# Kernel optimization log

Hardware: AMD Instinct MI355X
Metric: run time of the kernel (lower is better)

The kernel has to match this reference:

```python
import jax, jax.numpy as jnp
import numpy as np

N_USERS = 50000
N_ITEMS = 40000
D = 64
E = 1_000_000
NB = 3       # behaviors
L = 2        # GCN layers per behavior
B = 8192
N_NODES = (N_USERS + 1) + (N_ITEMS + 1)
REG_WEIGHT = 0.01
CL_TEMP = 0.1
BPR_GAMMA = 1e-10


def setup_inputs() -> dict:
    key = jax.random.key(0)
    k1, k2, k3, k4, k5 = jax.random.split(key, 5)
    user_emb = jax.random.normal(k1, (N_USERS + 1, D), jnp.float32) * 0.1
    item_emb = jax.random.normal(k2, (N_ITEMS + 1, D), jnp.float32) * 0.1
    gcn_w = jax.random.normal(k3, (NB, L, D, D), jnp.float32) * 0.1
    gcn_b = jnp.zeros((NB, L, D), jnp.float32)
    edge_index = jax.random.randint(k4, (NB, 2, E), 0, N_NODES, dtype=jnp.int64)
    batch_data = jax.random.randint(k5, (B, NB, 3), 0, 40000, dtype=jnp.int64)
    return {"user_emb": user_emb, "item_emb": item_emb, "gcn_w": gcn_w,
            "gcn_b": gcn_b, "edge_index": edge_index, "batch_data": batch_data}


def gcn_layer(x, edge_index, W, b):
    # PyG GCNConv(add_self_loops=False): h = x @ W; out[col] += norm * h[row]; out += b
    row, col = edge_index[0], edge_index[1]
    n = x.shape[0]
    deg = jnp.zeros((n,), x.dtype).at[col].add(1.0)
    dinv = jnp.where(deg > 0, jax.lax.rsqrt(jnp.maximum(deg, 1.0)), 0.0)
    norm = dinv[row] * dinv[col]                    # [E]
    h = x @ W                                       # [N, D]
    msg = h[row] * norm[:, None]                    # [E, D] gather
    out = jnp.zeros_like(x).at[col].add(msg)        # scatter-add
    return out + b


def _cos(a, b):
    num = jnp.sum(a * b, axis=-1)
    den = jnp.maximum(jnp.linalg.norm(a, axis=-1) * jnp.linalg.norm(b, axis=-1), 1e-8)
    return num / den


def reference(user_emb, item_emb, gcn_w, gcn_b, edge_index, batch_data):
    total = jnp.concatenate([user_emb, item_emb], axis=0)   # [N_NODES, D]
    total_loss = jnp.float32(0.0)
    te = total
    for bi in range(NB):
        # gcn propagate for this behavior (eval: dropout is identity)
        le = te
        for l in range(L):
            le = gcn_layer(le, edge_index[bi], gcn_w[bi, l], gcn_b[bi, l])
        # F.normalize(dim=-1)
        le = le / jnp.maximum(jnp.linalg.norm(le, axis=-1, keepdims=True), 1e-12)
        te = le + te
        # losses for this behavior
        users = batch_data[:, bi, 0]
        items = batch_data[:, bi, 1:]                        # [B, 2]
        ue = te[:N_USERS + 1]
        ie = te[N_USERS + 1:]
        uf = ue[users]                                       # [B, D]
        itf = ie[items]                                      # [B, 2, D]
        pos, neg = itf[:, 0], itf[:, 1]
        # info-nce (cross-entropy over [pos, neg] cosine sims, label 0)
        logits = jnp.stack([_cos(uf, pos), _cos(uf, neg)], axis=1) / CL_TEMP
        cl_loss = jnp.mean(-jax.nn.log_softmax(logits, axis=-1)[:, 0])
        # BPR loss (weight per behavior = 1.0)
        scores = jnp.sum(uf[:, None, :] * itf, axis=2)       # [B, 2]
        bpr = jnp.mean(-jnp.log(BPR_GAMMA + jax.nn.sigmoid(scores[:, 0] - scores[:, 1])))
        total_loss = total_loss + bpr + cl_loss
    # EmbLoss: sum of L2 norms of the raw embedding tables / last table's rows
    emb_loss = (jnp.linalg.norm(user_emb) + jnp.linalg.norm(item_emb)) / item_emb.shape[0]
    return total_loss + REG_WEIGHT * emb_loss
```

## Files before the change

### kernel.cpp

```cpp
#include <hip/hip_runtime.h>
#include <hip/hip_fp16.h>
#include <math.h>

#define NU 50001
#define NI 40001
#define NNODES 90002
#define DD 64
#define EE 1000000
#define NBB 3
#define LL 2
#define BB 8192
#define STRIDE 40
#define QS 16.0f
#define T4U (NU * 16)
#define T4T (NNODES * 16)
#define NBIN 352
#define NPAD (NBIN * 256)
#define CHUNK 4096
#define NBLK 245

__global__ __launch_bounds__(512) void k_scatp(const int* __restrict__ edge,
                                               unsigned* __restrict__ binbufC,
                                               unsigned* __restrict__ Hcnt,
                                               unsigned* __restrict__ Hoff) {
    __shared__ unsigned posc[NBIN];
    __shared__ unsigned sc[512];
    __shared__ unsigned lb[CHUNK];
    int bi = blockIdx.y, blk = blockIdx.x, tid = threadIdx.x;
    for (int i = tid; i < NBIN; i += 512) posc[i] = 0;
    __syncthreads();
    const int* rowp = edge + (size_t)bi * 2 * EE;
    const int* colp = rowp + EE;
    int base = blk * CHUNK;
    unsigned pk[8], bn[8];
    #pragma unroll
    for (int k = 0; k < 8; k++) {
        int e = base + k * 512 + tid;
        if (e < EE) {
            unsigned c = (unsigned)colp[e];
            pk[k] = ((c & 255u) << 17) | (unsigned)rowp[e];
            bn[k] = c >> 8;
            atomicAdd(&posc[bn[k]], 1u);
        } else bn[k] = 0xFFFFFFFFu;
    }
    __syncthreads();
    unsigned v = (tid < NBIN) ? posc[tid] : 0u;
    sc[tid] = v;
    __syncthreads();
    #pragma unroll
    for (int o = 1; o < 512; o <<= 1) {
        unsigned u = (tid >= o) ? sc[tid - o] : 0u;
        __syncthreads();
        sc[tid] += u;
        __syncthreads();
    }
    if (tid < NBIN) {
        unsigned excl = sc[tid] - v;
        Hcnt[((size_t)bi * NBLK + blk) * NBIN + tid] = v;
        Hoff[((size_t)bi * NBLK + blk) * NBIN + tid] = excl;
        posc[tid] = excl;
    }
    __syncthreads();
    #pragma unroll
    for (int k = 0; k < 8; k++) {
        if (bn[k] != 0xFFFFFFFFu) {
            unsigned pos = atomicAdd(&posc[bn[k]], 1u);
            lb[pos] = pk[k];
        }
    }
    __syncthreads();
    uint4* d4 = (uint4*)(binbufC + ((size_t)bi * NBLK + blk) * CHUNK);
    const uint4* s4 = (const uint4*)lb;
    #pragma unroll
    for (int k = 0; k < CHUNK / 4 / 512; k++)
        d4[k * 512 + tid] = s4[k * 512 + tid];
}

__global__ __launch_bounds__(256) void k_bucket(const unsigned* __restrict__ Hcnt,
                                                const unsigned* __restrict__ Hoff,
                                                const unsigned* __restrict__ binbufC,
                                                unsigned* __restrict__ cnt3, unsigned* __restrict__ bucket3) {
    __shared__ unsigned lb[256 * STRIDE];
    __shared__ unsigned cl[256];
    __shared__ unsigned so[NBLK + 1];
    __shared__ unsigned bo[NBLK];
    __shared__ unsigned sc[256];
    int bi = blockIdx.y, bin = blockIdx.x, tid = threadIdx.x;
    cl[tid] = 0;
    unsigned v = 0;
    if (tid < NBLK) {
        v = Hcnt[((size_t)bi * NBLK + tid) * NBIN + bin];
        bo[tid] = Hoff[((size_t)bi * NBLK + tid) * NBIN + bin];
    }
    sc[tid] = v;
    __syncthreads();
    #pragma unroll
    for (int o = 1; o < 256; o <<= 1) {
        unsigned u = (tid >= o) ? sc[tid - o] : 0u;
        __syncthreads();
        sc[tid] += u;
        __syncthreads();
    }
    if (tid == 0) so[0] = 0;
    if (tid < NBLK) so[tid + 1] = sc[tid];
    __syncthreads();
    unsigned T = so[NBLK];
    for (unsigned i = tid; i < T; i += 256) {
        int lo = 0, hi = NBLK;
        while (hi - lo > 1) { int mid = (lo + hi) >> 1; if (so[mid] <= i) lo = mid; else hi = mid; }
        unsigned w = binbufC[((size_t)bi * NBLK + lo) * CHUNK + bo[lo] + (i - so[lo])];
        unsigned c = w >> 17;
        unsigned pos = atomicAdd(&cl[c], 1u);
        if (pos < STRIDE) lb[c * STRIDE + pos] = w & 0x1FFFFu;
    }
    __syncthreads();
    cnt3[(size_t)bi * NPAD + (size_t)bin * 256 + tid] = cl[tid];
    uint4* dst = (uint4*)(bucket3 + (size_t)bi * NPAD * STRIDE + (size_t)bin * 256 * STRIDE);
    const uint4* srcl = (const uint4*)lb;
    #pragma unroll
    for (int k = 0; k < (256 * STRIDE / 4) / 256; k++)
        dst[k * 256 + tid] = srcl[k * 256 + tid];
}

__global__ __launch_bounds__(256) void k_init(const float* __restrict__ user_emb,
                                              const float* __restrict__ item_emb,
                                              const unsigned* __restrict__ cnt0,
                                              float* __restrict__ te, unsigned* __restrict__ X8a,
                                              float* __restrict__ scal) {
    int i0 = blockIdx.x * 256 + threadIdx.x;
    int stride = gridDim.x * 256;
    float su = 0.f, si = 0.f;
    const float4* u4 = (const float4*)user_emb;
    const float4* i4 = (const float4*)item_emb;
    float4* t4 = (float4*)te;
    for (int i = i0; i < T4T; i += stride) {
        float4 v;
        if (i < T4U) { v = u4[i]; su += v.x * v.x + v.y * v.y + v.z * v.z + v.w * v.w; }
        else         { v = i4[i - T4U]; si += v.x * v.x + v.y * v.y + v.z * v.z + v.w * v.w; }
        t4[i] = v;
        unsigned d = cnt0[i >> 4];
        float q = (d ? rsqrtf((float)d) : 0.f) * QS;
        int p0 = __builtin_amdgcn_cvt_pk_fp8_f32(v.x * q, v.y * q, 0, false);
        p0 = __builtin_amdgcn_cvt_pk_fp8_f32(v.z * q, v.w * q, p0, true);
        X8a[i] = (unsigned)p0;
    }
    #pragma unroll
    for (int o = 32; o > 0; o >>= 1) { su += __shfl_down(su, o); si += __shfl_down(si, o); }
    __shared__ float lsu[4], lsi[4];
    int w = threadIdx.x >> 6;
    if ((threadIdx.x & 63) == 0) { lsu[w] = su; lsi[w] = si; }
    __syncthreads();
    if (threadIdx.x == 0) {
        atomicAdd(scal + 1, lsu[0] + lsu[1] + lsu[2] + lsu[3]);
        atomicAdd(scal + 2, lsi[0] + lsi[1] + lsi[2] + lsi[3]);
    }
}

__global__ __launch_bounds__(256) void k_agg(const unsigned* __restrict__ cnt,
                                             const unsigned* __restrict__ bucket,
                                             const uint2* __restrict__ X8in,
                                             __half* __restrict__ agg) {
    int t = blockIdx.x * 256 + threadIdx.x;
    int r = t >> 6;
    if (r >= NNODES) return;
    int lane = t & 63;
    int j2 = lane & 7;
    int hw = lane >> 3;
    unsigned d = cnt[r];
    unsigned dc = d < STRIDE ? d : STRIDE;
    const unsigned* bk = bucket + (size_t)r * STRIDE;
    unsigned a0 = (hw +  0 < dc) ? bk[hw +  0] : (unsigned)NNODES;
    unsigned a1 = (hw +  8 < dc) ? bk[hw +  8] : (unsigned)NNODES;
    unsigned a2 = (hw + 16 < dc) ? bk[hw + 16] : (unsigned)NNODES;
    unsigned a3 = (hw + 24 < dc) ? bk[hw + 24] : (unsigned)NNODES;
    uint2 w0 = X8in[(size_t)a0 * 8 + j2];
    uint2 w1 = X8in[(size_t)a1 * 8 + j2];
    uint2 w2 = X8in[(size_t)a2 * 8 + j2];
    uint2 w3 = X8in[(size_t)a3 * 8 + j2];
    float4 A = {0.f, 0.f, 0.f, 0.f}, Bv = {0.f, 0.f, 0.f, 0.f};
#define ACC8(W) { \
    A.x  += __builtin_amdgcn_cvt_f32_fp8((int)W.x, 0); \
    A.y  += __builtin_amdgcn_cvt_f32_fp8((int)W.x, 1); \
    A.z  += __builtin_amdgcn_cvt_f32_fp8((int)W.x, 2); \
    A.w  += __builtin_amdgcn_cvt_f32_fp8((int)W.x, 3); \
    Bv.x += __builtin_amdgcn_cvt_f32_fp8((int)W.y, 0); \
    Bv.y += __builtin_amdgcn_cvt_f32_fp8((int)W.y, 1); \
    Bv.z += __builtin_amdgcn_cvt_f32_fp8((int)W.y, 2); \
    Bv.w += __builtin_amdgcn_cvt_f32_fp8((int)W.y, 3); }
    ACC8(w0) ACC8(w1) ACC8(w2) ACC8(w3)
    for (unsigned i = hw + 32; i < dc; i += 8) {
        uint2 w = X8in[(size_t)bk[i] * 8 + j2];
        ACC8(w)
    }
#undef ACC8
    #pragma unroll
    for (int o = 8; o <= 32; o <<= 1) {
        A.x  += __shfl_xor(A.x, o);  A.y  += __shfl_xor(A.y, o);
        A.z  += __shfl_xor(A.z, o);  A.w  += __shfl_xor(A.w, o);
        Bv.x += __shfl_xor(Bv.x, o); Bv.y += __shfl_xor(Bv.y, o);
        Bv.z += __shfl_xor(Bv.z, o); Bv.w += __shfl_xor(Bv.w, o);
    }
    if (hw == 0) {
        union { __half2 h[4]; float4 f; } u;
        u.h[0] = __floats2half2_rn(A.x, A.y);
        u.h[1] = __floats2half2_rn(A.z, A.w);
        u.h[2] = __floats2half2_rn(Bv.x, Bv.y);
        u.h[3] = __floats2half2_rn(Bv.z, Bv.w);
        ((float4*)agg)[(size_t)r * 8 + j2] = u.f;
    }
}

template <int FUSE>
__global__ __launch_bounds__(256) void k_gemmE(const __half* __restrict__ agg, const float* __restrict__ W,
                                               const float* __restrict__ b, const unsigned* __restrict__ cnt,
                                               float* __restrict__ te, unsigned* __restrict__ X8out,
                                               const unsigned* __restrict__ cnt_next) {
    __shared__ float ws[64 * 64];
    __shared__ float xs[16][64];
    int tid = threadIdx.x;
    #pragma unroll
    for (int q = 0; q < 4; q++)
        ((float4*)ws)[tid + q * 256] = ((const float4*)W)[tid + q * 256];
    int r0 = blockIdx.x * 16;
    {
        int rr = r0 + (tid >> 4);
        int cc = (tid & 15) * 4;
        if (rr < NNODES) {
            uint2 u = ((const uint2*)agg)[(size_t)rr * 16 + (tid & 15)];
            union { unsigned u; __half2 h; } c0, c1;
            c0.u = u.x; c1.u = u.y;
            float2 f0 = __half22float2(c0.h);
            float2 f1 = __half22float2(c1.h);
            xs[tid >> 4][cc + 0] = f0.x; xs[tid >> 4][cc + 1] = f0.y;
            xs[tid >> 4][cc + 2] = f1.x; xs[tid >> 4][cc + 3] = f1.y;
        }
    }
    __syncthreads();
    int rloc = tid >> 4;
    int j = tid & 15;
    int d4 = j * 4;
    int row = r0 + rloc;
    if (row >= NNODES) return;
    float4 acc = {0.f, 0.f, 0.f, 0.f};
    #pragma unroll
    for (int k = 0; k < 64; k++) {
        float xv = xs[rloc][k];
        float4 wv = *(const float4*)&ws[k * 64 + d4];
        acc.x += xv * wv.x; acc.y += xv * wv.y;
        acc.z += xv * wv.z; acc.w += xv * wv.w;
    }
    unsigned d = cnt[row];
    float m = (d ? rsqrtf((float)d) : 0.f) * (1.0f / QS);
    float4 bb = ((const float4*)b)[j];
    float vx = acc.x * m + bb.x;
    float vy = acc.y * m + bb.y;
    float vz = acc.z * m + bb.z;
    float vw = acc.w * m + bb.w;
    if (FUSE == 0) {
        unsigned dn = cnt_next[row];
        float q = (dn ? rsqrtf((float)dn) : 0.f) * QS;
        int p0 = __builtin_amdgcn_cvt_pk_fp8_f32(vx * q, vy * q, 0, false);
        p0 = __builtin_amdgcn_cvt_pk_fp8_f32(vz * q, vw * q, p0, true);
        X8out[(size_t)row * 16 + j] = (unsigned)p0;
    } else {
        float s = vx * vx + vy * vy + vz * vz + vw * vw;
        #pragma unroll
        for (int o = 1; o <= 8; o <<= 1) s += __shfl_xor(s, o);
        float scale = 1.f / fmaxf(sqrtf(s), 1e-12f);
        float4* te4 = (float4*)te;
        float4 old = te4[(size_t)row * 16 + j];
        old.x += vx * scale; old.y += vy * scale;
        old.z += vz * scale; old.w += vw * scale;
        te4[(size_t)row * 16 + j] = old;
        if (X8out) {
            unsigned dn = cnt_next[row];
            float q = (dn ? rsqrtf((float)dn) : 0.f) * QS;
            int p0 = __builtin_amdgcn_cvt_pk_fp8_f32(old.x * q, old.y * q, 0, false);
            p0 = __builtin_amdgcn_cvt_pk_fp8_f32(old.z * q, old.w * q, p0, true);
            X8out[(size_t)row * 16 + j] = (unsigned)p0;
        }
    }
}

__global__ __launch_bounds__(256) void k_loss(const float* __restrict__ te, const int* __restrict__ batch,
                                              int bi, float* __restrict__ acc) {
    int t = blockIdx.x * 256 + threadIdx.x;
    int s = t >> 6;
    int lane = t & 63;
    if (s >= BB) return;
    const int* bd = &batch[s * (NBB * 3) + bi * 3];
    int u = bd[0], p = bd[1], n = bd[2];
    float uv = te[(size_t)u * DD + lane];
    float pv = te[(size_t)(NU + p) * DD + lane];
    float nv = te[(size_t)(NU + n) * DD + lane];
    float d_up = uv * pv, d_un = uv * nv;
    float s_u = uv * uv, s_p = pv * pv, s_n = nv * nv;
    for (int o = 32; o > 0; o >>= 1) {
        d_up += __shfl_xor(d_up, o);
        d_un += __shfl_xor(d_un, o);
        s_u  += __shfl_xor(s_u, o);
        s_p  += __shfl_xor(s_p, o);
        s_n  += __shfl_xor(s_n, o);
    }
    __shared__ float part[4];
    if (lane == 0) {
        float cosp = d_up / fmaxf(sqrtf(s_u) * sqrtf(s_p), 1e-8f);
        float cosn = d_un / fmaxf(sqrtf(s_u) * sqrtf(s_n), 1e-8f);
        float cl = log1pf(expf((cosn - cosp) * 10.0f));
        float sig = 1.f / (1.f + expf(-(d_up - d_un)));
        float bpr = -logf(1e-10f + sig);
        part[(threadIdx.x >> 6) & 3] = cl + bpr;
    }
    __syncthreads();
    if (threadIdx.x == 0)
        atomicAdd(acc, (part[0] + part[1] + part[2] + part[3]) * (1.0f / BB));
}

__global__ void k_final(const float* __restrict__ scal, float* __restrict__ out) {
    if (threadIdx.x == 0 && blockIdx.x == 0)
        out[0] = scal[0] + 0.01f * (sqrtf(scal[1]) + sqrtf(scal[2])) / 40001.0f;
}

extern "C" void kernel_launch(void* const* d_in, const int* in_sizes, int n_in,
                              void* d_out, int out_size, void* d_ws, size_t ws_size,
                              hipStream_t stream) {
    const float* user_emb = (const float*)d_in[0];
    const float* item_emb = (const float*)d_in[1];
    const float* gcn_w    = (const float*)d_in[2];
    const float* gcn_b    = (const float*)d_in[3];
    const int*   edge_idx = (const int*)d_in[4];
    const int*   batch    = (const int*)d_in[5];
    float* out = (float*)d_out;

    char* ws = (char*)d_ws;
    size_t off = 0;
    auto alloc = [&](size_t bytes) {
        void* p = ws + off;
        off = (off + bytes + 511) & ~(size_t)511;
        return p;
    };
    float*    te      = (float*)alloc((size_t)NNODES * DD * sizeof(float));
    __half*   agg     = (__half*)alloc((size_t)NNODES * DD * sizeof(__half));
    unsigned* X8a     = (unsigned*)alloc((size_t)(NNODES + 1) * 16 * sizeof(unsigned));
    unsigned* X8b     = (unsigned*)alloc((size_t)(NNODES + 1) * 16 * sizeof(unsigned));
    unsigned* cnt3    = (unsigned*)alloc((size_t)NBB * NPAD * sizeof(unsigned));
    unsigned* bucket3 = (unsigned*)alloc((size_t)NBB * NPAD * STRIDE * sizeof(unsigned));
    unsigned* binbufC = (unsigned*)alloc((size_t)NBB * NBLK * CHUNK * sizeof(unsigned));
    unsigned* Hcnt    = (unsigned*)alloc((size_t)NBB * NBLK * NBIN * sizeof(unsigned));
    unsigned* Hoff    = (unsigned*)alloc((size_t)NBB * NBLK * NBIN * sizeof(unsigned));
    float*    scal    = (float*)alloc(64 * sizeof(float));

    hipMemsetAsync(scal, 0, 64 * sizeof(float), stream);
    hipMemsetAsync(X8a + (size_t)NNODES * 16, 0, 64, stream);
    hipMemsetAsync(X8b + (size_t)NNODES * 16, 0, 64, stream);

    k_scatp <<<dim3(NBLK, NBB), 512, 0, stream>>>(edge_idx, binbufC, Hcnt, Hoff);
    k_bucket<<<dim3(NBIN, NBB), 256, 0, stream>>>(Hcnt, Hoff, binbufC, cnt3, bucket3);

    k_init<<<1024, 256, 0, stream>>>(user_emb, item_emb, cnt3, te, X8a, scal);

    const int gat_grid  = (NNODES * DD + 255) / 256;
    const int gemm_grid = (NNODES + 15) / 16;

    for (int bi = 0; bi < NBB; bi++) {
        const unsigned* cnt = cnt3 + (size_t)bi * NPAD;
        const unsigned* bucket = bucket3 + (size_t)bi * NPAD * STRIDE;
        const float* W0 = gcn_w + ((size_t)bi * LL + 0) * DD * DD;
        const float* b0 = gcn_b + ((size_t)bi * LL + 0) * DD;
        const float* W1 = gcn_w + ((size_t)bi * LL + 1) * DD * DD;
        const float* b1 = gcn_b + ((size_t)bi * LL + 1) * DD;

        k_agg<<<gat_grid, 256, 0, stream>>>(cnt, bucket, (const uint2*)X8a, agg);
        k_gemmE<0><<<gemm_grid, 256, 0, stream>>>(agg, W0, b0, cnt, nullptr, X8b, cnt);

        k_agg<<<gat_grid, 256, 0, stream>>>(cnt, bucket, (const uint2*)X8b, agg);
        unsigned* x8next = (bi < NBB - 1) ? X8a : nullptr;
        const unsigned* cnt_next = cnt3 + (size_t)((bi + 1) % NBB) * NPAD;
        k_gemmE<1><<<gemm_grid, 256, 0, stream>>>(agg, W1, b1, cnt, te, x8next, cnt_next);

        k_loss<<<(BB * 64) / 256, 256, 0, stream>>>(te, batch, bi, scal);
    }

    k_final<<<1, 64, 0, stream>>>(scal, out);
}
```

Baseline: 485.4 us.

## Fold two GCN layer weights into one GEMM and transpose histogram table

Because the propagation operator is linear, the two per-behavior layer weights are premultiplied (W0·W1) and the layer-0 bias is carried through the second aggregation as a per-row dinv-weighted sum times b0·W1. This removes one GEMM kernel per behavior: the first aggregation now writes fp8 directly at a new quantisation scale. A transpose kernel is added so the bucket kernel reads its histogram coalesced, and small precompute kernels build dinv and the fused weights. The risks are extra fp8 rounding error from the different scaling and the cost of several added small launches.

```diff
diff --git a/kernel.cpp b/kernel.cpp
--- a/kernel.cpp
+++ b/kernel.cpp
@@ -12,6 +12,7 @@
 #define BB 8192
 #define STRIDE 40
 #define QS 16.0f
+#define QS2 64.0f
 #define T4U (NU * 16)
 #define T4T (NNODES * 16)
 #define NBIN 352
@@ -19,10 +20,20 @@
 #define CHUNK 4096
 #define NBLK 245
 
+__device__ __forceinline__ void acc8(float4& A, float4& Bv, uint2 w) {
+    A.x  += __builtin_amdgcn_cvt_f32_fp8((int)w.x, 0);
+    A.y  += __builtin_amdgcn_cvt_f32_fp8((int)w.x, 1);
+    A.z  += __builtin_amdgcn_cvt_f32_fp8((int)w.x, 2);
+    A.w  += __builtin_amdgcn_cvt_f32_fp8((int)w.x, 3);
+    Bv.x += __builtin_amdgcn_cvt_f32_fp8((int)w.y, 0);
+    Bv.y += __builtin_amdgcn_cvt_f32_fp8((int)w.y, 1);
+    Bv.z += __builtin_amdgcn_cvt_f32_fp8((int)w.y, 2);
+    Bv.w += __builtin_amdgcn_cvt_f32_fp8((int)w.y, 3);
+}
+
 __global__ __launch_bounds__(512) void k_scatp(const int* __restrict__ edge,
                                                unsigned* __restrict__ binbufC,
-                                               unsigned* __restrict__ Hcnt,
-                                               unsigned* __restrict__ Hoff) {
+                                               unsigned* __restrict__ Htab) {
     __shared__ unsigned posc[NBIN];
     __shared__ unsigned sc[512];
     __shared__ unsigned lb[CHUNK];
@@ -56,8 +67,8 @@
     }
     if (tid < NBIN) {
         unsigned excl = sc[tid] - v;
-        Hcnt[((size_t)bi * NBLK + blk) * NBIN + tid] = v;
-        Hoff[((size_t)bi * NBLK + blk) * NBIN + tid] = excl;
+        Htab[(((size_t)bi * 2 + 0) * NBLK + blk) * NBIN + tid] = v;
+        Htab[(((size_t)bi * 2 + 1) * NBLK + blk) * NBIN + tid] = excl;
         posc[tid] = excl;
     }
     __syncthreads();
@@ -76,8 +87,21 @@
         d4[k * 512 + tid] = s4[k * 512 + tid];
 }
 
-__global__ __launch_bounds__(256) void k_bucket(const unsigned* __restrict__ Hcnt,
-                                                const unsigned* __restrict__ Hoff,
+__global__ __launch_bounds__(1024) void k_transp(const unsigned* __restrict__ in, unsigned* __restrict__ out) {
+    __shared__ unsigned t[32][33];
+    int z = blockIdx.z;
+    const unsigned* I = in + (size_t)z * NBLK * NBIN;
+    unsigned* O = out + (size_t)z * NBIN * NBLK;
+    int bin0 = blockIdx.x * 32, blk0 = blockIdx.y * 32;
+    int tx = threadIdx.x & 31, ty = threadIdx.x >> 5;
+    int bin = bin0 + tx, blk = blk0 + ty;
+    if (blk < NBLK && bin < NBIN) t[ty][tx] = I[(size_t)blk * NBIN + bin];
+    __syncthreads();
+    int obin = bin0 + ty, oblk = blk0 + tx;
+    if (obin < NBIN && oblk < NBLK) O[(size_t)obin * NBLK + oblk] = t[tx][ty];
+}
+
+__global__ __launch_bounds__(256) void k_bucket(const unsigned* __restrict__ HtabT,
                                                 const unsigned* __restrict__ binbufC,
                                                 unsigned* __restrict__ cnt3, unsigned* __restrict__ bucket3) {
     __shared__ unsigned lb[256 * STRIDE];
@@ -89,8 +113,8 @@
     cl[tid] = 0;
     unsigned v = 0;
     if (tid < NBLK) {
-        v = Hcnt[((size_t)bi * NBLK + tid) * NBIN + bin];
-        bo[tid] = Hoff[((size_t)bi * NBLK + tid) * NBIN + bin];
+        v = HtabT[(((size_t)bi * 2 + 0) * NBIN + bin) * NBLK + tid];
+        bo[tid] = HtabT[(((size_t)bi * 2 + 1) * NBIN + bin) * NBLK + tid];
     }
     sc[tid] = v;
     __syncthreads();
@@ -120,6 +144,44 @@
     #pragma unroll
     for (int k = 0; k < (256 * STRIDE / 4) / 256; k++)
         dst[k * 256 + tid] = srcl[k * 256 + tid];
+}
+
+__global__ __launch_bounds__(256) void k_dinv3(const unsigned* __restrict__ cnt3, float* __restrict__ dinv3) {
+    int i = blockIdx.x * 256 + threadIdx.x;
+    if (i < NBB * NPAD) { unsigned d = cnt3[i]; dinv3[i] = d ? rsqrtf((float)d) : 0.f; }
+}
+
+__global__ __launch_bounds__(256) void k_wprep(const float* __restrict__ gcn_w, const float* __restrict__ gcn_b,
+                                               float* __restrict__ W01, float* __restrict__ bW) {
+    __shared__ float w0[64 * 64], w1[64 * 64];
+    int bi = blockIdx.x, tid = threadIdx.x;
+    const float* W0 = gcn_w + ((size_t)bi * 2 + 0) * 4096;
+    const float* W1 = gcn_w + ((size_t)bi * 2 + 1) * 4096;
+    #pragma unroll
+    for (int k = 0; k < 4; k++) {
+        ((float4*)w0)[k * 256 + tid] = ((const float4*)W0)[k * 256 + tid];
+        ((float4*)w1)[k * 256 + tid] = ((const float4*)W1)[k * 256 + tid];
+    }
+    __syncthreads();
+    int i = tid & 63;
+    int jq = tid >> 6;
+    float acc[16];
+    #pragma unroll
+    for (int j = 0; j < 16; j++) acc[j] = 0.f;
+    for (int k = 0; k < 64; k++) {
+        float a = w0[i * 64 + k];
+        #pragma unroll
+        for (int j = 0; j < 16; j++) acc[j] += a * w1[k * 64 + jq * 16 + j];
+    }
+    float* O = W01 + (size_t)bi * 4096 + (size_t)i * 64 + jq * 16;
+    #pragma unroll
+    for (int j = 0; j < 16; j++) O[j] = acc[j];
+    if (tid < 64) {
+        const float* b0 = gcn_b + ((size_t)bi * 2 + 0) * 64;
+        float a = 0.f;
+        for (int k = 0; k < 64; k++) a += b0[k] * w1[k * 64 + tid];
+        bW[bi * 64 + tid] = a;
+    }
 }
 
 __global__ __launch_bounds__(256) void k_init(const float* __restrict__ user_emb,
@@ -153,6 +215,59 @@
     if (threadIdx.x == 0) {
         atomicAdd(scal + 1, lsu[0] + lsu[1] + lsu[2] + lsu[3]);
         atomicAdd(scal + 2, lsi[0] + lsi[1] + lsi[2] + lsi[3]);
+    }
+}
+
+__global__ __launch_bounds__(256) void k_agg1(const unsigned* __restrict__ cnt,
+                                              const unsigned* __restrict__ bucket,
+                                              const uint2* __restrict__ X8in,
+                                              const float* __restrict__ dinv,
+                                              unsigned* __restrict__ X8out,
+                                              float* __restrict__ sarr) {
+    int t = blockIdx.x * 256 + threadIdx.x;
+    int r = t >> 6;
+    if (r >= NNODES) return;
+    int lane = t & 63;
+    int j2 = lane & 7;
+    int hw = lane >> 3;
+    unsigned d = cnt[r];
+    unsigned dc = d < STRIDE ? d : STRIDE;
+    const unsigned* bk = bucket + (size_t)r * STRIDE;
+    unsigned a0 = (hw +  0 < dc) ? bk[hw +  0] : (unsigned)NNODES;
+    unsigned a1 = (hw +  8 < dc) ? bk[hw +  8] : (unsigned)NNODES;
+    unsigned a2 = (hw + 16 < dc) ? bk[hw + 16] : (unsigned)NNODES;
+    unsigned a3 = (hw + 24 < dc) ? bk[hw + 24] : (unsigned)NNODES;
+    uint2 w0 = X8in[(size_t)a0 * 8 + j2];
+    uint2 w1 = X8in[(size_t)a1 * 8 + j2];
+    uint2 w2 = X8in[(size_t)a2 * 8 + j2];
+    uint2 w3 = X8in[(size_t)a3 * 8 + j2];
+    float sa = dinv[a0] + dinv[a1] + dinv[a2] + dinv[a3];
+    float4 A = {0.f, 0.f, 0.f, 0.f}, Bv = {0.f, 0.f, 0.f, 0.f};
+    acc8(A, Bv, w0); acc8(A, Bv, w1); acc8(A, Bv, w2); acc8(A, Bv, w3);
+    for (unsigned i = hw + 32; i < dc; i += 8) {
+        unsigned a = bk[i];
+        uint2 w = X8in[(size_t)a * 8 + j2];
+        acc8(A, Bv, w);
+        sa += dinv[a];
+    }
+    #pragma unroll
+    for (int o = 8; o <= 32; o <<= 1) {
+        A.x  += __shfl_xor(A.x, o);  A.y  += __shfl_xor(A.y, o);
+        A.z  += __shfl_xor(A.z, o);  A.w  += __shfl_xor(A.w, o);
+        Bv.x += __shfl_xor(Bv.x, o); Bv.y += __shfl_xor(Bv.y, o);
+        Bv.z += __shfl_xor(Bv.z, o); Bv.w += __shfl_xor(Bv.w, o);
+        sa   += __shfl_xor(sa, o);
+    }
+    float dv = dinv[r];
+    if (hw == 0) {
+        float q2 = QS2 * dv * dv * (1.0f / QS);
+        int p0 = __builtin_amdgcn_cvt_pk_fp8_f32(A.x * q2, A.y * q2, 0, false);
+        p0 = __builtin_amdgcn_cvt_pk_fp8_f32(A.z * q2, A.w * q2, p0, true);
+        int p1 = __builtin_amdgcn_cvt_pk_fp8_f32(Bv.x * q2, Bv.y * q2, 0, false);
+        p1 = __builtin_amdgcn_cvt_pk_fp8_f32(Bv.z * q2, Bv.w * q2, p1, true);
+        uint2 pw; pw.x = (unsigned)p0; pw.y = (unsigned)p1;
+        ((uint2*)X8out)[(size_t)r * 8 + j2] = pw;
+        if (j2 == 0) sarr[r] = dv * sa;
     }
 }
 
@@ -178,21 +293,11 @@
     uint2 w2 = X8in[(size_t)a2 * 8 + j2];
     uint2 w3 = X8in[(size_t)a3 * 8 + j2];
     float4 A = {0.f, 0.f, 0.f, 0.f}, Bv = {0.f, 0.f, 0.f, 0.f};
-#define ACC8(W) { \
-    A.x  += __builtin_amdgcn_cvt_f32_fp8((int)W.x, 0); \
-    A.y  += __builtin_amdgcn_cvt_f32_fp8((int)W.x, 1); \
-    A.z  += __builtin_amdgcn_cvt_f32_fp8((int)W.x, 2); \
-    A.w  += __builtin_amdgcn_cvt_f32_fp8((int)W.x, 3); \
-    Bv.x += __builtin_amdgcn_cvt_f32_fp8((int)W.y, 0); \
-    Bv.y += __builtin_amdgcn_cvt_f32_fp8((int)W.y, 1); \
-    Bv.z += __builtin_amdgcn_cvt_f32_fp8((int)W.y, 2); \
-    Bv.w += __builtin_amdgcn_cvt_f32_fp8((int)W.y, 3); }
-    ACC8(w0) ACC8(w1) ACC8(w2) ACC8(w3)
+    acc8(A, Bv, w0); acc8(A, Bv, w1); acc8(A, Bv, w2); acc8(A, Bv, w3);
     for (unsigned i = hw + 32; i < dc; i += 8) {
         uint2 w = X8in[(size_t)bk[i] * 8 + j2];
-        ACC8(w)
-    }
-#undef ACC8
+        acc8(A, Bv, w);
+    }
     #pragma unroll
     for (int o = 8; o <= 32; o <<= 1) {
         A.x  += __shfl_xor(A.x, o);  A.y  += __shfl_xor(A.y, o);
@@ -210,9 +315,9 @@
     }
 }
 
-template <int FUSE>
-__global__ __launch_bounds__(256) void k_gemmE(const __half* __restrict__ agg, const float* __restrict__ W,
-                                               const float* __restrict__ b, const unsigned* __restrict__ cnt,
+__global__ __launch_bounds__(256) void k_gemmE(const __half* __restrict__ agg, const float* __restrict__ W01,
+                                               const float* __restrict__ bW, const float* __restrict__ b1,
+                                               const unsigned* __restrict__ cnt, const float* __restrict__ sarr,
                                                float* __restrict__ te, unsigned* __restrict__ X8out,
                                                const unsigned* __restrict__ cnt_next) {
     __shared__ float ws[64 * 64];
@@ -220,7 +325,7 @@
     int tid = threadIdx.x;
     #pragma unroll
     for (int q = 0; q < 4; q++)
-        ((float4*)ws)[tid + q * 256] = ((const float4*)W)[tid + q * 256];
+        ((float4*)ws)[tid + q * 256] = ((const float4*)W01)[tid + q * 256];
     int r0 = blockIdx.x * 16;
     {
         int rr = r0 + (tid >> 4);
@@ -250,35 +355,29 @@
         acc.z += xv * wv.z; acc.w += xv * wv.w;
     }
     unsigned d = cnt[row];
-    float m = (d ? rsqrtf((float)d) : 0.f) * (1.0f / QS);
-    float4 bb = ((const float4*)b)[j];
-    float vx = acc.x * m + bb.x;
-    float vy = acc.y * m + bb.y;
-    float vz = acc.z * m + bb.z;
-    float vw = acc.w * m + bb.w;
-    if (FUSE == 0) {
+    float m = (d ? rsqrtf((float)d) : 0.f) * (1.0f / QS2);
+    float sv = sarr[row];
+    float4 bwv = ((const float4*)bW)[j];
+    float4 b1v = ((const float4*)b1)[j];
+    float vx = acc.x * m + sv * bwv.x + b1v.x;
+    float vy = acc.y * m + sv * bwv.y + b1v.y;
+    float vz = acc.z * m + sv * bwv.z + b1v.z;
+    float vw = acc.w * m + sv * bwv.w + b1v.w;
+    float s = vx * vx + vy * vy + vz * vz + vw * vw;
+    #pragma unroll
+    for (int o = 1; o <= 8; o <<= 1) s += __shfl_xor(s, o);
+    float scale = 1.f / fmaxf(sqrtf(s), 1e-12f);
+    float4* te4 = (float4*)te;
+    float4 old = te4[(size_t)row * 16 + j];
+    old.x += vx * scale; old.y += vy * scale;
+    old.z += vz * scale; old.w += vw * scale;
+    te4[(size_t)row * 16 + j] = old;
+    if (X8out) {
         unsigned dn = cnt_next[row];
         float q = (dn ? rsqrtf((float)dn) : 0.f) * QS;
-        int p0 = __builtin_amdgcn_cvt_pk_fp8_f32(vx * q, vy * q, 0, false);
-        p0 = __builtin_amdgcn_cvt_pk_fp8_f32(vz * q, vw * q, p0, true);
+        int p0 = __builtin_amdgcn_cvt_pk_fp8_f32(old.x * q, old.y * q, 0, false);
+        p0 = __builtin_amdgcn_cvt_pk_fp8_f32(old.z * q, old.w * q, p0, true);
         X8out[(size_t)row * 16 + j] = (unsigned)p0;
-    } else {
-        float s = vx * vx + vy * vy + vz * vz + vw * vw;
-        #pragma unroll
-        for (int o = 1; o <= 8; o <<= 1) s += __shfl_xor(s, o);
-        float scale = 1.f / fmaxf(sqrtf(s), 1e-12f);
-        float4* te4 = (float4*)te;
-        float4 old = te4[(size_t)row * 16 + j];
-        old.x += vx * scale; old.y += vy * scale;
-        old.z += vz * scale; old.w += vw * scale;
-        te4[(size_t)row * 16 + j] = old;
-        if (X8out) {
-            unsigned dn = cnt_next[row];
-            float q = (dn ? rsqrtf((float)dn) : 0.f) * QS;
-            int p0 = __builtin_amdgcn_cvt_pk_fp8_f32(old.x * q, old.y * q, 0, false);
-            p0 = __builtin_amdgcn_cvt_pk_fp8_f32(old.z * q, old.w * q, p0, true);
-            X8out[(size_t)row * 16 + j] = (unsigned)p0;
-        }
     }
 }
 
@@ -344,18 +443,25 @@
     unsigned* X8a     = (unsigned*)alloc((size_t)(NNODES + 1) * 16 * sizeof(unsigned));
     unsigned* X8b     = (unsigned*)alloc((size_t)(NNODES + 1) * 16 * sizeof(unsigned));
     unsigned* cnt3    = (unsigned*)alloc((size_t)NBB * NPAD * sizeof(unsigned));
+    float*    dinv3   = (float*)alloc((size_t)NBB * NPAD * sizeof(float));
     unsigned* bucket3 = (unsigned*)alloc((size_t)NBB * NPAD * STRIDE * sizeof(unsigned));
     unsigned* binbufC = (unsigned*)alloc((size_t)NBB * NBLK * CHUNK * sizeof(unsigned));
-    unsigned* Hcnt    = (unsigned*)alloc((size_t)NBB * NBLK * NBIN * sizeof(unsigned));
-    unsigned* Hoff    = (unsigned*)alloc((size_t)NBB * NBLK * NBIN * sizeof(unsigned));
+    unsigned* Htab    = (unsigned*)alloc((size_t)NBB * 2 * NBLK * NBIN * sizeof(unsigned));
+    unsigned* HtabT   = (unsigned*)alloc((size_t)NBB * 2 * NBIN * NBLK * sizeof(unsigned));
+    float*    W01     = (float*)alloc((size_t)NBB * 4096 * sizeof(float));
+    float*    bW      = (float*)alloc((size_t)NBB * 64 * sizeof(float));
+    float*    sarr    = (float*)alloc((size_t)NNODES * sizeof(float));
     float*    scal    = (float*)alloc(64 * sizeof(float));
 
     hipMemsetAsync(scal, 0, 64 * sizeof(float), stream);
     hipMemsetAsync(X8a + (size_t)NNODES * 16, 0, 64, stream);
     hipMemsetAsync(X8b + (size_t)NNODES * 16, 0, 64, stream);
 
-    k_scatp <<<dim3(NBLK, NBB), 512, 0, stream>>>(edge_idx, binbufC, Hcnt, Hoff);
-    k_bucket<<<dim3(NBIN, NBB), 256, 0, stream>>>(Hcnt, Hoff, binbufC, cnt3, bucket3);
+    k_scatp <<<dim3(NBLK, NBB), 512, 0, stream>>>(edge_idx, binbufC, Htab);
+    k_transp<<<dim3((NBIN + 31) / 32, (NBLK + 31) / 32, NBB * 2), 1024, 0, stream>>>(Htab, HtabT);
+    k_bucket<<<dim3(NBIN, NBB), 256, 0, stream>>>(HtabT, binbufC, cnt3, bucket3);
+    k_dinv3 <<<(NBB * NPAD + 255) / 256, 256, 0, stream>>>(cnt3, dinv3);
+    k_wprep <<<NBB, 256, 0, stream>>>(gcn_w, gcn_b, W01, bW);
 
     k_init<<<1024, 256, 0, stream>>>(user_emb, item_emb, cnt3, te, X8a, scal);
 
@@ -364,19 +470,16 @@
 
     for (int bi = 0; bi < NBB; bi++) {
         const unsigned* cnt = cnt3 + (size_t)bi * NPAD;
+        const float*    dnv = dinv3 + (size_t)bi * NPAD;
         const unsigned* bucket = bucket3 + (size_t)bi * NPAD * STRIDE;
-        const float* W0 = gcn_w + ((size_t)bi * LL + 0) * DD * DD;
-        const float* b0 = gcn_b + ((size_t)bi * LL + 0) * DD;
-        const float* W1 = gcn_w + ((size_t)bi * LL + 1) * DD * DD;
         const float* b1 = gcn_b + ((size_t)bi * LL + 1) * DD;
 
-        k_agg<<<gat_grid, 256, 0, stream>>>(cnt, bucket, (const uint2*)X8a, agg);
-        k_gemmE<0><<<gemm_grid, 256, 0, stream>>>(agg, W0, b0, cnt, nullptr, X8b, cnt);
-
+        k_agg1<<<gat_grid, 256, 0, stream>>>(cnt, bucket, (const uint2*)X8a, dnv, X8b, sarr);
         k_agg<<<gat_grid, 256, 0, stream>>>(cnt, bucket, (const uint2*)X8b, agg);
         unsigned* x8next = (bi < NBB - 1) ? X8a : nullptr;
         const unsigned* cnt_next = cnt3 + (size_t)((bi + 1) % NBB) * NPAD;
-        k_gemmE<1><<<gemm_grid, 256, 0, stream>>>(agg, W1, b1, cnt, te, x8next, cnt_next);
+        k_gemmE<<<gemm_grid, 256, 0, stream>>>(agg, W01 + (size_t)bi * 4096, bW + (size_t)bi * 64,
+                                               b1, cnt, sarr, te, x8next, cnt_next);
 
         k_loss<<<(BB * 64) / 256, 256, 0, stream>>>(te, batch, bi, scal);
     }
```

Result: faster. 441.1 us (-9.1%).
